# Optimization experiments

Measured on AMD Instinct MI355X. Metric: run time of the kernel, lower is better.

Reference implementation:

```python
import jax, jax.numpy as jnp
import numpy as np

N_EMBD = 1024
N_HEAD = 16
HEAD_SIZE = N_EMBD // N_HEAD
SEQ_LEN = 2048


def setup_inputs() -> dict:
    key = jax.random.key(0)
    k_x, k_wa, k_ba, k_wp, k_bp = jax.random.split(key, 5)
    s = 0.02
    return {
        "x": jax.random.normal(k_x, (4, SEQ_LEN, N_EMBD), dtype=jnp.float32),
        "w_attn": jax.random.normal(k_wa, (N_EMBD, 3 * N_EMBD), dtype=jnp.float32) * s,
        "b_attn": jax.random.normal(k_ba, (3 * N_EMBD,), dtype=jnp.float32) * s,
        "w_proj": jax.random.normal(k_wp, (N_EMBD, N_EMBD), dtype=jnp.float32) * s,
        "b_proj": jax.random.normal(k_bp, (N_EMBD,), dtype=jnp.float32) * s,
    }


def reference(x, w_attn, b_attn, w_proj, b_proj):
    B, T, C = x.shape
    H, D = N_HEAD, HEAD_SIZE
    qkv = x @ w_attn + b_attn                      # [B,T,3C]
    q, k, v = jnp.split(qkv, 3, axis=-1)
    q = q.reshape(B, T, H, D).transpose(0, 2, 1, 3)  # [B,H,T,D]
    k = k.reshape(B, T, H, D).transpose(0, 2, 1, 3)
    v = v.reshape(B, T, H, D).transpose(0, 2, 1, 3)
    att = jnp.einsum('bhqd,bhkd->bhqk', q, k) / jnp.sqrt(jnp.float32(D))
    causal = jnp.tril(jnp.ones((T, T), dtype=bool))
    att = jnp.where(causal[None, None], att, jnp.float32(-jnp.inf))
    att = jax.nn.softmax(att, axis=-1)
    out = jnp.einsum('bhqk,bhkd->bhqd', att, v)    # [B,H,T,D]
    out = out.transpose(0, 2, 1, 3).reshape(B, T, C)
    return out @ w_proj + b_proj
```

## Files before the change

kernel.cpp:

```cpp
#include <hip/hip_runtime.h>

typedef short short8 __attribute__((ext_vector_type(8)));
typedef short short4v __attribute__((ext_vector_type(4)));
typedef float f32x4 __attribute__((ext_vector_type(4)));
typedef unsigned uint2v __attribute__((ext_vector_type(2)));

__device__ __forceinline__ float bf2f(short b) {
  unsigned u = ((unsigned)(unsigned short)b) << 16;
  return __builtin_bit_cast(float, u);
}
__device__ __forceinline__ short f2bf(float f) {
  unsigned u = __builtin_bit_cast(unsigned, f);
  u += 0x7fffu + ((u >> 16) & 1u);
  return (short)(u >> 16);
}
__device__ __forceinline__ unsigned cvt_pk_bf16(float lo, float hi) {
  unsigned r;
  asm("v_cvt_pk_bf16_f32 %0, %1, %2" : "=v"(r) : "v"(lo), "v"(hi));
  return r;
}

__device__ __forceinline__ void gload_lds16(const void* g, void* l) {
  __builtin_amdgcn_global_load_lds(
      (const __attribute__((address_space(1))) unsigned int*)g,
      (__attribute__((address_space(3))) unsigned int*)l, 16, 0, 0);
}

__device__ __forceinline__ short8 lds_frag(const short* tile, int row, int kc, int l4) {
  int chunk = (kc * 4 + l4) ^ (row & 7);
  return *(const short8*)&tile[row * 64 + chunk * 8];
}

__global__ __launch_bounds__(256) void k_convert_bf16(const float* __restrict__ in,
                                                      short* __restrict__ out, int n8) {
  int i = blockIdx.x * 256 + threadIdx.x;
  if (i >= n8) return;
  const float4* p = (const float4*)in;
  float4 a = p[2 * i], b = p[2 * i + 1];
  short8 o;
  o[0] = f2bf(a.x); o[1] = f2bf(a.y); o[2] = f2bf(a.z); o[3] = f2bf(a.w);
  o[4] = f2bf(b.x); o[5] = f2bf(b.y); o[6] = f2bf(b.z); o[7] = f2bf(b.w);
  ((short8*)out)[i] = o;
}

__global__ __launch_bounds__(256) void k_transpose_w(const float* __restrict__ w,
                                                     short* __restrict__ wT, int K, int N) {
  __shared__ float t[32][33];
  int nt = N >> 5;
  int rt = blockIdx.x / nt, ct = blockIdx.x % nt;
  int tx = threadIdx.x & 31, ty = threadIdx.x >> 5;
#pragma unroll
  for (int i = 0; i < 4; ++i) {
    int r = ty * 4 + i;
    t[r][tx] = w[(size_t)(rt * 32 + r) * N + ct * 32 + tx];
  }
  __syncthreads();
#pragma unroll
  for (int i = 0; i < 4; ++i) {
    int r = ty * 4 + i;
    wT[(size_t)(ct * 32 + r) * K + rt * 32 + tx] = f2bf(t[tx][r]);
  }
}

template <bool BF16OUT>
__global__ __launch_bounds__(512, 1) void k_gemm8p(const short* __restrict__ A,
                                                   const short* __restrict__ Bt,
                                                   const float* __restrict__ bias,
                                                   void* __restrict__ Cout,
                                                   short* __restrict__ vTout,
                                                   int M, int N, int K) {
  __shared__ __align__(16) short Ab[2][256 * 64];
  __shared__ __align__(16) short Bb[2][128 * 64];
  int nt = N >> 7;
  int nwg = gridDim.x;
  int bid = blockIdx.x;
  int swz = (bid & 7) * (nwg >> 3) + (bid >> 3);
  int mt = swz / nt, ct = swz % nt;
  int tid = threadIdx.x, w = tid >> 6, lane = tid & 63;
  int l15 = lane & 15, l4 = lane >> 4;
  int wm = w >> 2, wn = w & 3;
  const short* Abase = A + (size_t)mt * 256 * K;
  const short* Bbase = Bt + (size_t)ct * 128 * K;
  int NT = K >> 6;

  int srow = lane >> 3;
  int slc = (lane & 7) ^ srow;

  auto stage = [&](const short* gbase, short* dstTile, int kt, int half) {
#pragma unroll
    for (int i = 0; i < 2; ++i) {
      int rowg = half * 128 + i * 64 + w * 8;
      gload_lds16(gbase + (size_t)(rowg + srow) * K + kt * 64 + slc * 8,
                  dstTile + (size_t)rowg * 64);
    }
  };

  f32x4 acc[8][2];
#pragma unroll
  for (int m = 0; m < 8; ++m)
#pragma unroll
    for (int n = 0; n < 2; ++n) acc[m][n] = f32x4{0.f, 0.f, 0.f, 0.f};

  stage(Bbase, &Bb[0][0], 0, 0);
  stage(Abase, &Ab[0][0], 0, 0);
  stage(Abase, &Ab[0][0], 0, 1);
  stage(Bbase, &Bb[1][0], 1, 0);
  stage(Abase, &Ab[1][0], 1, 0);
  asm volatile("s_waitcnt vmcnt(6)" ::: "memory");
  __builtin_amdgcn_s_barrier();

  for (int t = 0; t < NT; ++t) {
    int b = t & 1;
    const short* At = &Ab[b][0];
    const short* Btl = &Bb[b][0];
    bool p1 = (t + 1 < NT), p2 = (t + 2 < NT);

    short8 alo[4][2], ahi[4][2], bfr[2][2];

#pragma unroll
    for (int mq = 0; mq < 4; ++mq)
#pragma unroll
      for (int kc = 0; kc < 2; ++kc)
        alo[mq][kc] = lds_frag(At, wm * 128 + mq * 16 + l15, kc, l4);
#pragma unroll
    for (int n = 0; n < 2; ++n)
#pragma unroll
      for (int kc = 0; kc < 2; ++kc)
        bfr[n][kc] = lds_frag(Btl, wn * 32 + n * 16 + l15, kc, l4);
    if (p1) stage(Abase, &Ab[(t + 1) & 1][0], t + 1, 1);
    __builtin_amdgcn_s_barrier();
    asm volatile("s_waitcnt lgkmcnt(0)" ::: "memory");
    __builtin_amdgcn_sched_barrier(0);
    __builtin_amdgcn_s_setprio(1);
#pragma unroll
    for (int mq = 0; mq < 4; ++mq)
#pragma unroll
      for (int n = 0; n < 2; ++n)
#pragma unroll
        for (int kc = 0; kc < 2; ++kc)
          acc[mq][n] = __builtin_amdgcn_mfma_f32_16x16x32_bf16(alo[mq][kc], bfr[n][kc], acc[mq][n], 0, 0, 0);
    __builtin_amdgcn_s_setprio(0);
    if (p1) {
      asm volatile("s_waitcnt vmcnt(6)" ::: "memory");
    } else {
      asm volatile("s_waitcnt vmcnt(0)" ::: "memory");
    }
    __builtin_amdgcn_s_barrier();

#pragma unroll
    for (int mq = 0; mq < 4; ++mq)
#pragma unroll
      for (int kc = 0; kc < 2; ++kc)
        ahi[mq][kc] = lds_frag(At, wm * 128 + 64 + mq * 16 + l15, kc, l4);
    if (p2) {
      stage(Bbase, &Bb[b][0], t + 2, 0);
      stage(Abase, &Ab[b][0], t + 2, 0);
    }
    __builtin_amdgcn_s_barrier();
    asm volatile("s_waitcnt lgkmcnt(0)" ::: "memory");
    __builtin_amdgcn_sched_barrier(0);
    __builtin_amdgcn_s_setprio(1);
#pragma unroll
    for (int mq = 0; mq < 4; ++mq)
#pragma unroll
      for (int n = 0; n < 2; ++n)
#pragma unroll
        for (int kc = 0; kc < 2; ++kc)
          acc[4 + mq][n] = __builtin_amdgcn_mfma_f32_16x16x32_bf16(ahi[mq][kc], bfr[n][kc], acc[4 + mq][n], 0, 0, 0);
    __builtin_amdgcn_s_setprio(0);
    if (p2) {
      asm volatile("s_waitcnt vmcnt(6)" ::: "memory");
    } else if (p1) {
      asm volatile("s_waitcnt vmcnt(2)" ::: "memory");
    }
    __builtin_amdgcn_s_barrier();
  }

#pragma unroll
  for (int m = 0; m < 8; ++m) {
#pragma unroll
    for (int n = 0; n < 2; ++n) {
      int row = mt * 256 + wm * 128 + m * 16 + l4 * 4;
      int col = ct * 128 + wn * 32 + n * 16 + l15;
      float bv = bias[col];
      if constexpr (BF16OUT) {
        short4v pk4;
#pragma unroll
        for (int j = 0; j < 4; ++j) pk4[j] = f2bf(acc[m][n][j] + bv);
        if (col >= 2048) {
          int hh = (col - 2048) >> 6, dd = (col - 2048) & 63;
          int batch2 = row >> 11, tok = row & 2047;
          *(short4v*)(vTout + (((size_t)(batch2 * 16 + hh) * 64 + dd) << 11) + tok) = pk4;
        } else {
#pragma unroll
          for (int j = 0; j < 4; ++j)
            ((short*)Cout)[(size_t)(row + j) * N + col] = pk4[j];
        }
      } else {
#pragma unroll
        for (int j = 0; j < 4; ++j)
          ((float*)Cout)[(size_t)(row + j) * N + col] = acc[m][n][j] + bv;
      }
    }
  }
}

__global__ __launch_bounds__(256, 2) void k_attn(const short* __restrict__ qkv,
                                                 const short* __restrict__ vT,
                                                 short* __restrict__ out) {
  constexpr int T = 2048, C3 = 3072;
  __shared__ __align__(16) short Kl[2][64 * 72];
  __shared__ __align__(16) short P_lds[4][2][32 * 72];
  int i_ = blockIdx.x;
  int xcd = i_ & 7, m_ = i_ >> 3;
  int bh = xcd * 8 + (m_ & 7), bp = m_ >> 3;
  int batch = bh >> 4, h = bh & 15;
  int tid = threadIdx.x, w = tid >> 6, lane = tid & 63;
  int l15 = lane & 15, l4 = lane >> 4;

  int qt[2];
  qt[0] = 63 - (bp * 4 + w);
  qt[1] = bp * 4 + w;
  int lim[2] = {qt[0] >> 1, qt[1] >> 1};
  int ktb = (63 - bp * 4) >> 1;

  const short* kbase = qkv + (size_t)(batch * T) * C3 + 1024 + h * 64;
  const short* vbase = vT + (size_t)bh * 64 * T;

  int sr0 = tid >> 3, sr1 = 32 + (tid >> 3), sdc = (tid & 7) * 8;

  const float SCL = 0.18033688f;
  short8 qf[2][2][2];
#pragma unroll
  for (int t = 0; t < 2; ++t)
#pragma unroll
    for (int qc = 0; qc < 2; ++qc) {
      const short* qrow = qkv + (size_t)(batch * T + qt[t] * 32 + qc * 16 + l15) * C3 + h * 64;
#pragma unroll
      for (int kc = 0; kc < 2; ++kc) {
        short8 v = *(const short8*)(qrow + kc * 32 + l4 * 8);
#pragma unroll
        for (int i = 0; i < 8; ++i) v[i] = f2bf(bf2f(v[i]) * SCL);
        qf[t][qc][kc] = v;
      }
    }

  const f32x4 ZERO = f32x4{0.f, 0.f, 0.f, 0.f};
  short8 ONES;
#pragma unroll
  for (int i = 0; i < 8; ++i) ONES[i] = (short)0x3F80;

  f32x4 o_[2][2][4];
  f32x4 lacc[2][2];
#pragma unroll
  for (int t = 0; t < 2; ++t)
#pragma unroll
    for (int qc = 0; qc < 2; ++qc) {
      lacc[t][qc] = ZERO;
#pragma unroll
      for (int dt = 0; dt < 4; ++dt) o_[t][qc][dt] = ZERO;
    }

  {
    short8 a = *(const short8*)(kbase + (size_t)sr0 * C3 + sdc);
    short8 b = *(const short8*)(kbase + (size_t)sr1 * C3 + sdc);
    *(short8*)&Kl[0][sr0 * 72 + sdc] = a;
    *(short8*)&Kl[0][sr1 * 72 + sdc] = b;
  }
  __syncthreads();

  int cur = 0;
  for (int kt = 0; kt <= ktb; ++kt) {
    bool more = (kt < ktb);
    bool act0 = (kt <= lim[0]), act1 = (kt <= lim[1]);

    short8 pre0, pre1;
    if (more) {
      pre0 = *(const short8*)(kbase + (size_t)((kt + 1) * 64 + sr0) * C3 + sdc);
      pre1 = *(const short8*)(kbase + (size_t)((kt + 1) * 64 + sr1) * C3 + sdc);
    }

    const short* Kb = &Kl[cur][0];
    short8 kf[4][2];
#pragma unroll
    for (int kvt = 0; kvt < 4; ++kvt)
#pragma unroll
      for (int kc = 0; kc < 2; ++kc)
        kf[kvt][kc] = *(const short8*)(Kb + (kvt * 16 + l15) * 72 + kc * 32 + l4 * 8);

    short8 vf[4][2];
#pragma unroll
    for (int dt = 0; dt < 4; ++dt)
#pragma unroll
      for (int kc = 0; kc < 2; ++kc)
        vf[dt][kc] = *(const short8*)(vbase + (size_t)(dt * 16 + l15) * T + kt * 64 + kc * 32 + l4 * 8);

#pragma unroll
    for (int t = 0; t < 2; ++t) {
      bool act = (t == 0) ? act0 : act1;
      if (!act) continue;
      short* pb = &P_lds[w][t][0];

#pragma unroll
      for (int qc = 0; qc < 2; ++qc) {
        f32x4 s[4];
        __builtin_amdgcn_s_setprio(1);
#pragma unroll
        for (int kvt = 0; kvt < 4; ++kvt) {
          s[kvt] = __builtin_amdgcn_mfma_f32_16x16x32_bf16(kf[kvt][0], qf[t][qc][0], ZERO, 0, 0, 0);
          s[kvt] = __builtin_amdgcn_mfma_f32_16x16x32_bf16(kf[kvt][1], qf[t][qc][1], s[kvt], 0, 0, 0);
        }
        __builtin_amdgcn_s_setprio(0);

        if (kt == lim[t]) {
          int qg = qt[t] * 32 + qc * 16 + l15;
#pragma unroll
          for (int kvt = 0; kvt < 4; ++kvt)
#pragma unroll
            for (int j = 0; j < 4; ++j) {
              int kg = kt * 64 + kvt * 16 + l4 * 4 + j;
              if (kg > qg) s[kvt][j] = -1e30f;
            }
        }

#pragma unroll
        for (int kvt = 0; kvt < 4; ++kvt) {
          float p0 = exp2f(s[kvt][0]);
          float p1 = exp2f(s[kvt][1]);
          float p2 = exp2f(s[kvt][2]);
          float p3 = exp2f(s[kvt][3]);
          unsigned lo = cvt_pk_bf16(p0, p1);
          unsigned hi = cvt_pk_bf16(p2, p3);
          *(uint2v*)(pb + (qc * 16 + l15) * 72 + kvt * 16 + l4 * 4) = uint2v{lo, hi};
        }
      }
    }

    asm volatile("s_waitcnt lgkmcnt(0)" ::: "memory");

    __builtin_amdgcn_s_setprio(1);
#pragma unroll
    for (int t = 0; t < 2; ++t) {
      bool act = (t == 0) ? act0 : act1;
      if (!act) continue;
      const short* pb = &P_lds[w][t][0];
#pragma unroll
      for (int qc = 0; qc < 2; ++qc)
#pragma unroll
        for (int kc = 0; kc < 2; ++kc) {
          short8 pf = *(const short8*)(pb + (qc * 16 + l15) * 72 + kc * 32 + l4 * 8);
          lacc[t][qc] = __builtin_amdgcn_mfma_f32_16x16x32_bf16(ONES, pf, lacc[t][qc], 0, 0, 0);
#pragma unroll
          for (int dt = 0; dt < 4; ++dt)
            o_[t][qc][dt] = __builtin_amdgcn_mfma_f32_16x16x32_bf16(vf[dt][kc], pf, o_[t][qc][dt], 0, 0, 0);
        }
    }
    __builtin_amdgcn_s_setprio(0);

    if (more) {
      *(short8*)&Kl[cur ^ 1][sr0 * 72 + sdc] = pre0;
      *(short8*)&Kl[cur ^ 1][sr1 * 72 + sdc] = pre1;
    }
    __syncthreads();
    cur ^= 1;
  }

#pragma unroll
  for (int t = 0; t < 2; ++t) {
#pragma unroll
    for (int qc = 0; qc < 2; ++qc) {
      float inv = 1.f / lacc[t][qc][0];
      size_t rowb = (size_t)(batch * T + qt[t] * 32 + qc * 16 + l15) * 1024 + h * 64;
#pragma unroll
      for (int dt = 0; dt < 4; ++dt) {
        short4v pk4;
#pragma unroll
        for (int j = 0; j < 4; ++j) pk4[j] = f2bf(o_[t][qc][dt][j] * inv);
        *(short4v*)(out + rowb + dt * 16 + l4 * 4) = pk4;
      }
    }
  }
}

extern "C" void kernel_launch(void* const* d_in, const int* in_sizes, int n_in,
                              void* d_out, int out_size, void* d_ws, size_t ws_size,
                              hipStream_t stream) {
  const float* x      = (const float*)d_in[0];
  const float* w_attn = (const float*)d_in[1];
  const float* b_attn = (const float*)d_in[2];
  const float* w_proj = (const float*)d_in[3];
  const float* b_proj = (const float*)d_in[4];
  float* out = (float*)d_out;

  char* ws = (char*)d_ws;
  short* xb   = (short*)(ws);
  short* waT  = (short*)(ws + 16777216);
  short* wpT  = (short*)(ws + 23068672);
  short* qkv  = (short*)(ws + 25165824);
  short* vT   = (short*)(ws + 75497472);
  short* attn = xb;

  k_convert_bf16<<<4096, 256, 0, stream>>>(x, xb, 1048576);
  k_transpose_w<<<32 * 96, 256, 0, stream>>>(w_attn, waT, 1024, 3072);
  k_transpose_w<<<32 * 32, 256, 0, stream>>>(w_proj, wpT, 1024, 1024);
  k_gemm8p<true><<<768, 512, 0, stream>>>(xb, waT, b_attn, qkv, vT, 8192, 3072, 1024);
  k_attn<<<512, 256, 0, stream>>>(qkv, vT, attn);
  k_gemm8p<false><<<256, 512, 0, stream>>>(attn, wpT, b_proj, out, nullptr, 8192, 1024, 1024);
}
```

Baseline: 186.9 us.

## Split attention q-tile pairs across 8 waves instead of 4 per block

The attention kernel now launches 512 threads per block. Each of 8 waves handles one 32-row query tile, where previously 4 waves each handled a paired long and short tile. Per-wave register state for Q, O and the row sums is halved, and launch bounds ask for 4 blocks per CU to raise occupancy. V fragments are now loaded only for active waves and after QK, so waves done with the causal region skip that global traffic. The cost is that finished short-tile waves sit idle at barriers while the long-tile waves continue, and each K tile load is shared by more waves.

Result: slower. 229.4 us (+22.7%).

```diff
diff --git a/kernel.cpp b/kernel.cpp
--- a/kernel.cpp
+++ b/kernel.cpp
@@ -205,12 +205,12 @@
   }
 }
 
-__global__ __launch_bounds__(256, 2) void k_attn(const short* __restrict__ qkv,
+__global__ __launch_bounds__(512, 4) void k_attn(const short* __restrict__ qkv,
                                                  const short* __restrict__ vT,
                                                  short* __restrict__ out) {
   constexpr int T = 2048, C3 = 3072;
   __shared__ __align__(16) short Kl[2][64 * 72];
-  __shared__ __align__(16) short P_lds[4][2][32 * 72];
+  __shared__ __align__(16) short P_lds[8][32 * 72];
   int i_ = blockIdx.x;
   int xcd = i_ & 7, m_ = i_ >> 3;
   int bh = xcd * 8 + (m_ & 7), bp = m_ >> 3;
@@ -218,88 +218,67 @@
   int tid = threadIdx.x, w = tid >> 6, lane = tid & 63;
   int l15 = lane & 15, l4 = lane >> 4;
 
-  int qt[2];
-  qt[0] = 63 - (bp * 4 + w);
-  qt[1] = bp * 4 + w;
-  int lim[2] = {qt[0] >> 1, qt[1] >> 1};
+  int qt = (w < 4) ? (63 - (bp * 4 + w)) : (bp * 4 + (w - 4));
+  int lim = qt >> 1;
   int ktb = (63 - bp * 4) >> 1;
 
   const short* kbase = qkv + (size_t)(batch * T) * C3 + 1024 + h * 64;
   const short* vbase = vT + (size_t)bh * 64 * T;
 
-  int sr0 = tid >> 3, sr1 = 32 + (tid >> 3), sdc = (tid & 7) * 8;
+  int sr = tid >> 3, sdc = (tid & 7) * 8;
 
   const float SCL = 0.18033688f;
-  short8 qf[2][2][2];
-#pragma unroll
-  for (int t = 0; t < 2; ++t)
-#pragma unroll
-    for (int qc = 0; qc < 2; ++qc) {
-      const short* qrow = qkv + (size_t)(batch * T + qt[t] * 32 + qc * 16 + l15) * C3 + h * 64;
-#pragma unroll
-      for (int kc = 0; kc < 2; ++kc) {
-        short8 v = *(const short8*)(qrow + kc * 32 + l4 * 8);
-#pragma unroll
-        for (int i = 0; i < 8; ++i) v[i] = f2bf(bf2f(v[i]) * SCL);
-        qf[t][qc][kc] = v;
-      }
-    }
+  short8 qf[2][2];
+#pragma unroll
+  for (int qc = 0; qc < 2; ++qc) {
+    const short* qrow = qkv + (size_t)(batch * T + qt * 32 + qc * 16 + l15) * C3 + h * 64;
+#pragma unroll
+    for (int kc = 0; kc < 2; ++kc) {
+      short8 v = *(const short8*)(qrow + kc * 32 + l4 * 8);
+#pragma unroll
+      for (int i = 0; i < 8; ++i) v[i] = f2bf(bf2f(v[i]) * SCL);
+      qf[qc][kc] = v;
+    }
+  }
 
   const f32x4 ZERO = f32x4{0.f, 0.f, 0.f, 0.f};
   short8 ONES;
 #pragma unroll
   for (int i = 0; i < 8; ++i) ONES[i] = (short)0x3F80;
 
-  f32x4 o_[2][2][4];
-  f32x4 lacc[2][2];
-#pragma unroll
-  for (int t = 0; t < 2; ++t)
-#pragma unroll
-    for (int qc = 0; qc < 2; ++qc) {
-      lacc[t][qc] = ZERO;
-#pragma unroll
-      for (int dt = 0; dt < 4; ++dt) o_[t][qc][dt] = ZERO;
-    }
+  f32x4 o_[2][4];
+  f32x4 lacc[2];
+#pragma unroll
+  for (int qc = 0; qc < 2; ++qc) {
+    lacc[qc] = ZERO;
+#pragma unroll
+    for (int dt = 0; dt < 4; ++dt) o_[qc][dt] = ZERO;
+  }
 
   {
-    short8 a = *(const short8*)(kbase + (size_t)sr0 * C3 + sdc);
-    short8 b = *(const short8*)(kbase + (size_t)sr1 * C3 + sdc);
-    *(short8*)&Kl[0][sr0 * 72 + sdc] = a;
-    *(short8*)&Kl[0][sr1 * 72 + sdc] = b;
+    short8 a = *(const short8*)(kbase + (size_t)sr * C3 + sdc);
+    *(short8*)&Kl[0][sr * 72 + sdc] = a;
   }
   __syncthreads();
 
+  short* pb = &P_lds[w][0];
   int cur = 0;
   for (int kt = 0; kt <= ktb; ++kt) {
     bool more = (kt < ktb);
-    bool act0 = (kt <= lim[0]), act1 = (kt <= lim[1]);
-
-    short8 pre0, pre1;
-    if (more) {
-      pre0 = *(const short8*)(kbase + (size_t)((kt + 1) * 64 + sr0) * C3 + sdc);
-      pre1 = *(const short8*)(kbase + (size_t)((kt + 1) * 64 + sr1) * C3 + sdc);
-    }
-
-    const short* Kb = &Kl[cur][0];
-    short8 kf[4][2];
-#pragma unroll
-    for (int kvt = 0; kvt < 4; ++kvt)
-#pragma unroll
-      for (int kc = 0; kc < 2; ++kc)
-        kf[kvt][kc] = *(const short8*)(Kb + (kvt * 16 + l15) * 72 + kc * 32 + l4 * 8);
-
-    short8 vf[4][2];
-#pragma unroll
-    for (int dt = 0; dt < 4; ++dt)
-#pragma unroll
-      for (int kc = 0; kc < 2; ++kc)
-        vf[dt][kc] = *(const short8*)(vbase + (size_t)(dt * 16 + l15) * T + kt * 64 + kc * 32 + l4 * 8);
-
-#pragma unroll
-    for (int t = 0; t < 2; ++t) {
-      bool act = (t == 0) ? act0 : act1;
-      if (!act) continue;
-      short* pb = &P_lds[w][t][0];
+    bool act = (kt <= lim);
+
+    short8 pre;
+    if (more)
+      pre = *(const short8*)(kbase + (size_t)((kt + 1) * 64 + sr) * C3 + sdc);
+
+    if (act) {
+      const short* Kb = &Kl[cur][0];
+      short8 kf[4][2];
+#pragma unroll
+      for (int kvt = 0; kvt < 4; ++kvt)
+#pragma unroll
+        for (int kc = 0; kc < 2; ++kc)
+          kf[kvt][kc] = *(const short8*)(Kb + (kvt * 16 + l15) * 72 + kc * 32 + l4 * 8);
 
 #pragma unroll
       for (int qc = 0; qc < 2; ++qc) {
@@ -307,13 +286,13 @@
         __builtin_amdgcn_s_setprio(1);
 #pragma unroll
         for (int kvt = 0; kvt < 4; ++kvt) {
-          s[kvt] = __builtin_amdgcn_mfma_f32_16x16x32_bf16(kf[kvt][0], qf[t][qc][0], ZERO, 0, 0, 0);
-          s[kvt] = __builtin_amdgcn_mfma_f32_16x16x32_bf16(kf[kvt][1], qf[t][qc][1], s[kvt], 0, 0, 0);
+          s[kvt] = __builtin_amdgcn_mfma_f32_16x16x32_bf16(kf[kvt][0], qf[qc][0], ZERO, 0, 0, 0);
+          s[kvt] = __builtin_amdgcn_mfma_f32_16x16x32_bf16(kf[kvt][1], qf[qc][1], s[kvt], 0, 0, 0);
         }
         __builtin_amdgcn_s_setprio(0);
 
-        if (kt == lim[t]) {
-          int qg = qt[t] * 32 + qc * 16 + l15;
+        if (kt == lim) {
+          int qg = qt * 32 + qc * 16 + l15;
 #pragma unroll
           for (int kvt = 0; kvt < 4; ++kvt)
 #pragma unroll
@@ -334,50 +313,47 @@
           *(uint2v*)(pb + (qc * 16 + l15) * 72 + kvt * 16 + l4 * 4) = uint2v{lo, hi};
         }
       }
-    }
-
-    asm volatile("s_waitcnt lgkmcnt(0)" ::: "memory");
-
-    __builtin_amdgcn_s_setprio(1);
-#pragma unroll
-    for (int t = 0; t < 2; ++t) {
-      bool act = (t == 0) ? act0 : act1;
-      if (!act) continue;
-      const short* pb = &P_lds[w][t][0];
+
+      short8 vf[4][2];
+#pragma unroll
+      for (int dt = 0; dt < 4; ++dt)
+#pragma unroll
+        for (int kc = 0; kc < 2; ++kc)
+          vf[dt][kc] = *(const short8*)(vbase + (size_t)(dt * 16 + l15) * T + kt * 64 + kc * 32 + l4 * 8);
+
+      asm volatile("s_waitcnt lgkmcnt(0)" ::: "memory");
+
+      __builtin_amdgcn_s_setprio(1);
 #pragma unroll
       for (int qc = 0; qc < 2; ++qc)
 #pragma unroll
         for (int kc = 0; kc < 2; ++kc) {
           short8 pf = *(const short8*)(pb + (qc * 16 + l15) * 72 + kc * 32 + l4 * 8);
-          lacc[t][qc] = __builtin_amdgcn_mfma_f32_16x16x32_bf16(ONES, pf, lacc[t][qc], 0, 0, 0);
+          lacc[qc] = __builtin_amdgcn_mfma_f32_16x16x32_bf16(ONES, pf, lacc[qc], 0, 0, 0);
 #pragma unroll
           for (int dt = 0; dt < 4; ++dt)
-            o_[t][qc][dt] = __builtin_amdgcn_mfma_f32_16x16x32_bf16(vf[dt][kc], pf, o_[t][qc][dt], 0, 0, 0);
-        }
-    }
-    __builtin_amdgcn_s_setprio(0);
+            o_[qc][dt] = __builtin_amdgcn_mfma_f32_16x16x32_bf16(vf[dt][kc], pf, o_[qc][dt], 0, 0, 0);
+        }
+      __builtin_amdgcn_s_setprio(0);
+    }
 
     if (more) {
-      *(short8*)&Kl[cur ^ 1][sr0 * 72 + sdc] = pre0;
-      *(short8*)&Kl[cur ^ 1][sr1 * 72 + sdc] = pre1;
+      *(short8*)&Kl[cur ^ 1][sr * 72 + sdc] = pre;
     }
     __syncthreads();
     cur ^= 1;
   }
 
 #pragma unroll
-  for (int t = 0; t < 2; ++t) {
-#pragma unroll
-    for (int qc = 0; qc < 2; ++qc) {
-      float inv = 1.f / lacc[t][qc][0];
-      size_t rowb = (size_t)(batch * T + qt[t] * 32 + qc * 16 + l15) * 1024 + h * 64;
-#pragma unroll
-      for (int dt = 0; dt < 4; ++dt) {
-        short4v pk4;
-#pragma unroll
-        for (int j = 0; j < 4; ++j) pk4[j] = f2bf(o_[t][qc][dt][j] * inv);
-        *(short4v*)(out + rowb + dt * 16 + l4 * 4) = pk4;
-      }
+  for (int qc = 0; qc < 2; ++qc) {
+    float inv = 1.f / lacc[qc][0];
+    size_t rowb = (size_t)(batch * T + qt * 32 + qc * 16 + l15) * 1024 + h * 64;
+#pragma unroll
+    for (int dt = 0; dt < 4; ++dt) {
+      short4v pk4;
+#pragma unroll
+      for (int j = 0; j < 4; ++j) pk4[j] = f2bf(o_[qc][dt][j] * inv);
+      *(short4v*)(out + rowb + dt * 16 + l4 * 4) = pk4;
     }
   }
 }
@@ -404,6 +380,6 @@
   k_transpose_w<<<32 * 96, 256, 0, stream>>>(w_attn, waT, 1024, 3072);
   k_transpose_w<<<32 * 32, 256, 0, stream>>>(w_proj, wpT, 1024, 1024);
   k_gemm8p<true><<<768, 512, 0, stream>>>(xb, waT, b_attn, qkv, vT, 8192, 3072, 1024);
-  k_attn<<<512, 256, 0, stream>>>(qkv, vT, attn);
+  k_attn<<<512, 512, 0, stream>>>(qkv, vT, attn);
   k_gemm8p<false><<<256, 512, 0, stream>>>(attn, wpT, b_proj, out, nullptr, 8192, 1024, 1024);
 }
```

## Use 256x256-tile two-phase pipelined GEMM for QKV projection

Applied to the files above, without the earlier changes.

Adds a new GEMM kernel that computes 256x256 output tiles per workgroup, up from 256x128, and uses it for the QKV projection with half as many workgroups. The K loop is split into two phases over the upper and lower A halves, with staggered global-to-LDS prefetches, s_setprio around the MFMA blocks, and explicit vmcnt waits to overlap loads with compute. The larger tile raises operand reuse and arithmetic intensity. In exchange it uses more LDS (128 KB) and more accumulator registers, and 384 workgroups on 256 CUs leaves an uneven tail wave.

Result: slower. 190.9 us (+2.1%).

```diff
diff --git a/kernel.cpp b/kernel.cpp
--- a/kernel.cpp
+++ b/kernel.cpp
@@ -59,6 +59,152 @@
   for (int i = 0; i < 4; ++i) {
     int r = ty * 4 + i;
     wT[(size_t)(ct * 32 + r) * K + rt * 32 + tx] = f2bf(t[tx][r]);
+  }
+}
+
+template <bool BF16OUT>
+__global__ __launch_bounds__(512, 1) void k_gemm2ph256(const short* __restrict__ A,
+                                                       const short* __restrict__ Bt,
+                                                       const float* __restrict__ bias,
+                                                       void* __restrict__ Cout,
+                                                       short* __restrict__ vTout,
+                                                       int M, int N, int K) {
+  __shared__ __align__(16) short Ab[2][256 * 64];
+  __shared__ __align__(16) short Bb[2][256 * 64];
+  int nt = N >> 8;
+  int nwg = gridDim.x;
+  int bid = blockIdx.x;
+  int swz = (bid & 7) * (nwg >> 3) + (bid >> 3);
+  int mt = swz / nt, ct = swz % nt;
+  int tid = threadIdx.x, w = tid >> 6, lane = tid & 63;
+  int l15 = lane & 15, l4 = lane >> 4;
+  int wm = w >> 2, wn = w & 3;
+  const short* Abase = A + (size_t)mt * 256 * K;
+  const short* Bbase = Bt + (size_t)ct * 256 * K;
+  int NT = K >> 6;
+
+  int srow = lane >> 3;
+  int slc = (lane & 7) ^ srow;
+
+  auto stage = [&](const short* gbase, short* dstTile, int kt, int half) {
+#pragma unroll
+    for (int i = 0; i < 2; ++i) {
+      int rowg = half * 128 + i * 64 + w * 8;
+      gload_lds16(gbase + (size_t)(rowg + srow) * K + kt * 64 + slc * 8,
+                  dstTile + (size_t)rowg * 64);
+    }
+  };
+
+  f32x4 acc[8][4];
+#pragma unroll
+  for (int m = 0; m < 8; ++m)
+#pragma unroll
+    for (int n = 0; n < 4; ++n) acc[m][n] = f32x4{0.f, 0.f, 0.f, 0.f};
+
+  stage(Bbase, &Bb[0][0], 0, 0);
+  stage(Bbase, &Bb[0][0], 0, 1);
+  stage(Abase, &Ab[0][0], 0, 0);
+  stage(Abase, &Ab[0][0], 0, 1);
+  stage(Bbase, &Bb[1][0], 1, 0);
+  stage(Bbase, &Bb[1][0], 1, 1);
+  stage(Abase, &Ab[1][0], 1, 0);
+  asm volatile("s_waitcnt vmcnt(6)" ::: "memory");
+  __builtin_amdgcn_s_barrier();
+
+  for (int t = 0; t < NT; ++t) {
+    int b = t & 1;
+    const short* At = &Ab[b][0];
+    const short* Btl = &Bb[b][0];
+    bool p1 = (t + 1 < NT), p2 = (t + 2 < NT);
+
+    short8 alo[4][2], ahi[4][2], bfr[4][2];
+
+#pragma unroll
+    for (int mq = 0; mq < 4; ++mq)
+#pragma unroll
+      for (int kc = 0; kc < 2; ++kc)
+        alo[mq][kc] = lds_frag(At, wm * 128 + mq * 16 + l15, kc, l4);
+#pragma unroll
+    for (int nq = 0; nq < 4; ++nq)
+#pragma unroll
+      for (int kc = 0; kc < 2; ++kc)
+        bfr[nq][kc] = lds_frag(Btl, wn * 64 + nq * 16 + l15, kc, l4);
+    if (p1) stage(Abase, &Ab[(t + 1) & 1][0], t + 1, 1);
+    __builtin_amdgcn_s_barrier();
+    asm volatile("s_waitcnt lgkmcnt(0)" ::: "memory");
+    __builtin_amdgcn_sched_barrier(0);
+    __builtin_amdgcn_s_setprio(1);
+#pragma unroll
+    for (int mq = 0; mq < 4; ++mq)
+#pragma unroll
+      for (int nq = 0; nq < 4; ++nq)
+#pragma unroll
+        for (int kc = 0; kc < 2; ++kc)
+          acc[mq][nq] = __builtin_amdgcn_mfma_f32_16x16x32_bf16(alo[mq][kc], bfr[nq][kc], acc[mq][nq], 0, 0, 0);
+    __builtin_amdgcn_s_setprio(0);
+    if (p1) {
+      asm volatile("s_waitcnt vmcnt(8)" ::: "memory");
+    } else {
+      asm volatile("s_waitcnt vmcnt(0)" ::: "memory");
+    }
+    __builtin_amdgcn_s_barrier();
+
+#pragma unroll
+    for (int mq = 0; mq < 4; ++mq)
+#pragma unroll
+      for (int kc = 0; kc < 2; ++kc)
+        ahi[mq][kc] = lds_frag(At, wm * 128 + 64 + mq * 16 + l15, kc, l4);
+    if (p2) {
+      stage(Bbase, &Bb[b][0], t + 2, 0);
+      stage(Bbase, &Bb[b][0], t + 2, 1);
+      stage(Abase, &Ab[b][0], t + 2, 0);
+    }
+    __builtin_amdgcn_s_barrier();
+    asm volatile("s_waitcnt lgkmcnt(0)" ::: "memory");
+    __builtin_amdgcn_sched_barrier(0);
+    __builtin_amdgcn_s_setprio(1);
+#pragma unroll
+    for (int mq = 0; mq < 4; ++mq)
+#pragma unroll
+      for (int nq = 0; nq < 4; ++nq)
+#pragma unroll
+        for (int kc = 0; kc < 2; ++kc)
+          acc[4 + mq][nq] = __builtin_amdgcn_mfma_f32_16x16x32_bf16(ahi[mq][kc], bfr[nq][kc], acc[4 + mq][nq], 0, 0, 0);
+    __builtin_amdgcn_s_setprio(0);
+    if (p2) {
+      asm volatile("s_waitcnt vmcnt(8)" ::: "memory");
+    } else if (p1) {
+      asm volatile("s_waitcnt vmcnt(2)" ::: "memory");
+    }
+    __builtin_amdgcn_s_barrier();
+  }
+
+#pragma unroll
+  for (int m = 0; m < 8; ++m) {
+#pragma unroll
+    for (int n = 0; n < 4; ++n) {
+      int row = mt * 256 + wm * 128 + m * 16 + l4 * 4;
+      int col = ct * 256 + wn * 64 + n * 16 + l15;
+      float bv = bias[col];
+      if constexpr (BF16OUT) {
+        short4v pk4;
+#pragma unroll
+        for (int j = 0; j < 4; ++j) pk4[j] = f2bf(acc[m][n][j] + bv);
+        if (col >= 2048) {
+          int hh = (col - 2048) >> 6, dd = (col - 2048) & 63;
+          int batch2 = row >> 11, tok = row & 2047;
+          *(short4v*)(vTout + (((size_t)(batch2 * 16 + hh) * 64 + dd) << 11) + tok) = pk4;
+        } else {
+#pragma unroll
+          for (int j = 0; j < 4; ++j)
+            ((short*)Cout)[(size_t)(row + j) * N + col] = pk4[j];
+        }
+      } else {
+#pragma unroll
+        for (int j = 0; j < 4; ++j)
+          ((float*)Cout)[(size_t)(row + j) * N + col] = acc[m][n][j] + bv;
+      }
+    }
   }
 }
 
@@ -403,7 +549,7 @@
   k_convert_bf16<<<4096, 256, 0, stream>>>(x, xb, 1048576);
   k_transpose_w<<<32 * 96, 256, 0, stream>>>(w_attn, waT, 1024, 3072);
   k_transpose_w<<<32 * 32, 256, 0, stream>>>(w_proj, wpT, 1024, 1024);
-  k_gemm8p<true><<<768, 512, 0, stream>>>(xb, waT, b_attn, qkv, vT, 8192, 3072, 1024);
+  k_gemm2ph256<true><<<384, 512, 0, stream>>>(xb, waT, b_attn, qkv, vT, 8192, 3072, 1024);
   k_attn<<<512, 256, 0, stream>>>(qkv, vT, attn);
   k_gemm8p<false><<<256, 512, 0, stream>>>(attn, wpT, b_proj, out, nullptr, 8192, 1024, 1024);
 }
```
